# Kernel tuning notes

Measured on AMD Instinct MI355X. Metric: run time of the kernel, lower is better.

The kernel has to match this reference:

```python
import jax, jax.numpy as jnp
import numpy as np
import math

_PI = math.pi

@jax.custom_vjp
def atan_spike(h):
    # Heaviside forward, ATan surrogate (alpha=2.0) backward
    return (h >= 0).astype(h.dtype)

def _atan_fwd(h):
    return (h >= 0).astype(h.dtype), h

def _atan_bwd(h, g):
    # d/dh [ (1/pi) atan(pi*h) + 1/2 ] = 1 / (1 + (pi*h)^2)
    return (g / (1.0 + (_PI * h) ** 2),)

atan_spike.defvjp(_atan_fwd, _atan_bwd)

def plif_scan(x, alpha, v_th):
    # x: [T, ...]; PLIF: v += alpha*(x - v); spike; hard reset to 0
    a = alpha.reshape(())
    def step(v, xt):
        v = v + a * (xt - v)
        s = atan_spike(v - v_th)
        v = v * (1.0 - s)
        return v, s
    v0 = jnp.zeros_like(x[0])
    _, spikes = jax.lax.scan(step, v0, x)
    return spikes

def setup_inputs() -> dict:
    key = jax.random.key(0)
    k1, k2, k3 = jax.random.split(key, 3)
    T, B, N, D, H = 4, 8, 1024, 512, 2048
    x = jax.random.normal(k1, (T, B, N, D), dtype=jnp.float32)
    W1 = jax.random.normal(k2, (H, D), dtype=jnp.float32) * (1.0 / math.sqrt(D))
    W2 = jax.random.normal(k3, (D, H), dtype=jnp.float32) * (1.0 / math.sqrt(H))
    alpha1 = jnp.full((1,), 0.5, dtype=jnp.float32)  # 1/tau, tau=2.0
    alpha2 = jnp.full((1,), 0.5, dtype=jnp.float32)
    return {"x": x, "W1": W1, "W2": W2, "alpha1": alpha1, "alpha2": alpha2}

def reference(x, W1, W2, alpha1, alpha2):
    V_TH = 1.0
    h = jnp.einsum('tbnd,hd->tbnh', x, W1)      # fc1 (no bias)
    s1 = plif_scan(h, alpha1, V_TH)             # PLIF neuron 1
    y = jnp.einsum('tbnh,dh->tbnd', s1, W2)     # fc2 (no bias)
    s2 = plif_scan(y, alpha2, V_TH)             # PLIF neuron 2
    return s2
```

## Files before the change

### kernel.cpp

```cpp
#include <hip/hip_runtime.h>

#define T_  4
#define BN_ 8192
#define D_  512
#define H_  2048

typedef float f4 __attribute__((ext_vector_type(4)));
typedef float f32x4 __attribute__((ext_vector_type(4)));
typedef _Float16 f16x8 __attribute__((ext_vector_type(8)));

__device__ __forceinline__ void split8(const f4 u0, const f4 u1, f16x8& hi, f16x8& lo) {
#pragma unroll
    for (int i = 0; i < 4; ++i) {
        _Float16 a = (_Float16)u0[i]; hi[i]     = a; lo[i]     = (_Float16)(u0[i] - (float)a);
        _Float16 b = (_Float16)u1[i]; hi[4 + i] = b; lo[4 + i] = (_Float16)(u1[i] - (float)b);
    }
}

__device__ __forceinline__ void spikes4_to_f16(unsigned b, unsigned& lo, unsigned& hi) {
    const unsigned p0 = (b & 0xFFu) | ((b & 0xFF00u) << 8);
    const unsigned p1 = ((b >> 16) & 0xFFu) | ((b >> 8) & 0xFF0000u);
    lo = p0 * 0x3C00u;
    hi = p1 * 0x3C00u;
}

__device__ __forceinline__ void glds16(const void* g, void* l) {
    __builtin_amdgcn_global_load_lds((const __attribute__((address_space(1))) unsigned int*)g,
                                     (__attribute__((address_space(3))) unsigned int*)l, 16, 0, 0);
}

__global__ __launch_bounds__(256)
void k_split(const float* __restrict__ x, _Float16* __restrict__ xs)
{
    const int b     = blockIdx.x;
    const int t     = b & 3;
    const int k0B   = (b >> 2) & 15;
    const int bnB64 = b >> 6;
    const int kg    = threadIdx.x & 3;
    const int row64 = threadIdx.x >> 2;

    const float* src = x + ((size_t)t * BN_ + bnB64 * 64 + row64) * D_ + k0B * 32 + kg * 8;
    const f4 u0 = *(const f4*)src;
    const f4 u1 = *(const f4*)(src + 4);
    f16x8 hi, lo;
    split8(u0, u1, hi, lo);

    const int bnB32 = bnB64 * 2 + (row64 >> 5);
    const int r     = row64 & 31;
    const size_t base = (size_t)(bnB32 * 16 + k0B) * 8192 + t * 2048;
    *(f16x8*)&xs[base +        kg * 256 + r * 8] = hi;
    *(f16x8*)&xs[base + 1024 + kg * 256 + r * 8] = lo;
}

__global__ __launch_bounds__(256)
void k_splitW(const float* __restrict__ W1, _Float16* __restrict__ w1s)
{
    const int gid = blockIdx.x * 256 + threadIdx.x;
    const int col = gid & 127;
    const int kg  = (gid >> 7) & 3;
    const int kb  = (gid >> 9) & 15;
    const int h0b = gid >> 13;

    const float* src = W1 + (size_t)(h0b * 128 + col) * D_ + kb * 32 + kg * 8;
    const f4 u0 = *(const f4*)src;
    const f4 u1 = *(const f4*)(src + 4);
    f16x8 hi, lo;
    split8(u0, u1, hi, lo);

    const size_t base = (size_t)(h0b * 16 + kb) * 8192;
    *(f16x8*)&w1s[base +        kg * 1024 + col * 8] = hi;
    *(f16x8*)&w1s[base + 4096 + kg * 1024 + col * 8] = lo;
}

__global__ __launch_bounds__(256)
void k_splitW2(const float* __restrict__ W2, _Float16* __restrict__ w2s)
{
    const int gid = blockIdx.x * 256 + threadIdx.x;
    const int col = gid & 127;
    const int kg  = (gid >> 7) & 3;
    const int kb  = (gid >> 9) & 63;
    const int d0b = gid >> 15;

    const float* src = W2 + (size_t)(d0b * 128 + col) * H_ + kb * 32 + kg * 8;
    const f4 u0 = *(const f4*)src;
    const f4 u1 = *(const f4*)(src + 4);
    f16x8 hi, lo;
    split8(u0, u1, hi, lo);

    const size_t base = (size_t)(d0b * 64 + kb) * 8192;
    *(f16x8*)&w2s[base +        kg * 1024 + col * 8] = hi;
    *(f16x8*)&w2s[base + 4096 + kg * 1024 + col * 8] = lo;
}

__global__ __launch_bounds__(256, 4)
void k_fc1b(const _Float16* __restrict__ xs, const _Float16* __restrict__ w1s,
            const float* __restrict__ alphap, unsigned char* __restrict__ s1)
{
    __shared__ _Float16 Ab[2][T_][2][4][32][8];

    const int tid  = threadIdx.x;
    const int lane = tid & 63;
    const int w    = tid >> 6;
    const int wc   = w * 32;

    const int gid   = blockIdx.x;
    const int panel = gid >> 8;
    const int h0i   = (gid >> 4) & 15;
    const int bnL   = gid & 15;
    const int bnB   = panel * 16 + bnL;
    const int bn0   = bnB * 32;
    const int h0    = h0i * 128;

    const int l15 = lane & 15;
    const int kgl = lane >> 4;
    const int lq  = kgl * 4;

    const float a1v = alphap[0];

    f32x4 acc[T_][2][2];
#pragma unroll
    for (int t = 0; t < T_; ++t)
#pragma unroll
        for (int m = 0; m < 2; ++m)
#pragma unroll
            for (int n = 0; n < 2; ++n) acc[t][m][n] = (f32x4){0.f, 0.f, 0.f, 0.f};

    const char* xbase = (const char*)xs + (size_t)bnB * 16 * 16384;
    const _Float16* bl = w1s + (size_t)h0i * (16 * 8192)
                             + (size_t)kgl * 1024 + (size_t)(wc + l15) * 8;

#define FC1_GLDS(BUF, KB)                                                        \
    {                                                                            \
        const char* cb_ = xbase + (size_t)(KB) * 16384;                          \
        _Float16* lA_ = &Ab[BUF][0][0][0][0][0];                                 \
        _Pragma("unroll")                                                        \
        for (int i_ = 0; i_ < 4; ++i_) {                                         \
            const int s_ = i_ * 4 + w;                                           \
            glds16(cb_ + s_ * 1024 + lane * 16, lA_ + s_ * 512);                 \
        }                                                                        \
    }

#define FC1_BLOAD(KB, B0, B1)                                                    \
    {                                                                            \
        const _Float16* bp_ = bl + (size_t)(KB) * 8192;                          \
        B0[0] = *(const f16x8*)(bp_);                                            \
        B0[1] = *(const f16x8*)(bp_ + 128);                                      \
        B1[0] = *(const f16x8*)(bp_ + 4096);                                     \
        B1[1] = *(const f16x8*)(bp_ + 4096 + 128);                               \
    }

#define FC1_COMPUTE(BUF, B0, B1)                                                 \
    _Pragma("unroll")                                                            \
    for (int t_ = 0; t_ < T_; ++t_)                                              \
        _Pragma("unroll")                                                        \
        for (int m_ = 0; m_ < 2; ++m_) {                                         \
            const f16x8 a0_ = *(const f16x8*)&Ab[BUF][t_][0][kgl][m_ * 16 + l15][0]; \
            const f16x8 a1_ = *(const f16x8*)&Ab[BUF][t_][1][kgl][m_ * 16 + l15][0]; \
            _Pragma("unroll")                                                    \
            for (int n_ = 0; n_ < 2; ++n_) {                                     \
                acc[t_][m_][n_] = __builtin_amdgcn_mfma_f32_16x16x32_f16(a0_, B0[n_], acc[t_][m_][n_], 0, 0, 0); \
                acc[t_][m_][n_] = __builtin_amdgcn_mfma_f32_16x16x32_f16(a0_, B1[n_], acc[t_][m_][n_], 0, 0, 0); \
                acc[t_][m_][n_] = __builtin_amdgcn_mfma_f32_16x16x32_f16(a1_, B0[n_], acc[t_][m_][n_], 0, 0, 0); \
            }                                                                    \
        }

    f16x8 bA0[2], bA1[2], bB0[2], bB1[2];

    FC1_BLOAD(0, bA0, bA1)
    __builtin_amdgcn_sched_barrier(0);
    FC1_GLDS(0, 0)

#pragma unroll 1
    for (int it = 0; it < 8; ++it) {
        const int kb = 2 * it;
        __builtin_amdgcn_s_barrier();
        FC1_BLOAD(kb + 1, bB0, bB1)
        __builtin_amdgcn_sched_barrier(0);
        FC1_GLDS(1, kb + 1)
        asm volatile("s_waitcnt vmcnt(8)" ::: "memory");
        __builtin_amdgcn_sched_barrier(0);
        FC1_COMPUTE(0, bA0, bA1)
        __builtin_amdgcn_s_barrier();
        if (it < 7) {
            FC1_BLOAD(kb + 2, bA0, bA1)
            __builtin_amdgcn_sched_barrier(0);
            FC1_GLDS(0, kb + 2)
            asm volatile("s_waitcnt vmcnt(8)" ::: "memory");
        } else {
            asm volatile("s_waitcnt vmcnt(0)" ::: "memory");
        }
        __builtin_amdgcn_sched_barrier(0);
        FC1_COMPUTE(1, bB0, bB1)
    }

#pragma unroll
    for (int m = 0; m < 2; ++m)
#pragma unroll
        for (int n = 0; n < 2; ++n)
#pragma unroll
            for (int q = 0; q < 4; ++q) {
                float v = 0.f;
#pragma unroll
                for (int t = 0; t < T_; ++t) {
                    v = v + a1v * (acc[t][m][n][q] - v);
                    const bool sp = (v >= 1.0f);
                    s1[((size_t)t * BN_ + bn0 + m * 16 + lq + q) * H_ +
                       (h0 + wc + n * 16 + l15)] = sp ? (unsigned char)1 : (unsigned char)0;
                    if (sp) v = 0.f;
                }
            }
}

__global__ __launch_bounds__(256, 2)
void k_fc2b(const unsigned char* __restrict__ s1, const _Float16* __restrict__ w2s,
            const float* __restrict__ alphap, float* __restrict__ out)
{
    __shared__ _Float16 A2[2][T_][4][64][8];

    const int tid  = threadIdx.x;
    const int lane = tid & 63;
    const int w    = tid >> 6;
    const int wr   = (w >> 1) * 32;
    const int wc   = (w & 1) * 64;
    const int bn0  = blockIdx.x * 64;
    const int d0i  = blockIdx.y;
    const int d0   = d0i * 128;

    const int l15 = lane & 15;
    const int kgl = lane >> 4;
    const int lq  = kgl * 4;

    const int at   = w;
    const int arow = lane;

    const float a2v = alphap[0];

    f32x4 acc[T_][2][4];
#pragma unroll
    for (int t = 0; t < T_; ++t)
#pragma unroll
        for (int m = 0; m < 2; ++m)
#pragma unroll
            for (int n = 0; n < 4; ++n) acc[t][m][n] = (f32x4){0.f, 0.f, 0.f, 0.f};

    const unsigned char* ap = s1 + ((size_t)at * BN_ + bn0 + arow) * H_;
    const _Float16* bl = w2s + (size_t)d0i * (64 * 8192)
                             + (size_t)kgl * 1024 + (size_t)(wc + l15) * 8;

#define FC2_ACONV_WRITE(BUF, R0, R1)                                             \
    {                                                                            \
        unsigned v_[8];                                                          \
        spikes4_to_f16(R0.x, v_[0], v_[1]); spikes4_to_f16(R0.y, v_[2], v_[3]);  \
        spikes4_to_f16(R0.z, v_[4], v_[5]); spikes4_to_f16(R0.w, v_[6], v_[7]);  \
        *(uint4*)&A2[BUF][at][0][arow][0] = *(const uint4*)&v_[0];               \
        *(uint4*)&A2[BUF][at][1][arow][0] = *(const uint4*)&v_[4];               \
        spikes4_to_f16(R1.x, v_[0], v_[1]); spikes4_to_f16(R1.y, v_[2], v_[3]);  \
        spikes4_to_f16(R1.z, v_[4], v_[5]); spikes4_to_f16(R1.w, v_[6], v_[7]);  \
        *(uint4*)&A2[BUF][at][2][arow][0] = *(const uint4*)&v_[0];               \
        *(uint4*)&A2[BUF][at][3][arow][0] = *(const uint4*)&v_[4];               \
    }

#define FC2_BLOAD(KB, B0, B1)                                                    \
    {                                                                            \
        const _Float16* bp_ = bl + (size_t)(KB) * 8192;                          \
        _Pragma("unroll")                                                        \
        for (int n_ = 0; n_ < 4; ++n_) {                                         \
            B0[n_] = *(const f16x8*)(bp_ + n_ * 128);                            \
            B1[n_] = *(const f16x8*)(bp_ + 4096 + n_ * 128);                     \
        }                                                                        \
    }

    f16x8 bc0[4], bc1[4], bpA0[4], bpA1[4];

    {
        const uint4 r0 = *(const uint4*)(ap);
        const uint4 r1 = *(const uint4*)(ap + 16);
        FC2_ACONV_WRITE(0, r0, r1)
        FC2_BLOAD(0, bc0, bc1)
    }
    __syncthreads();

    int cur = 0;
    for (int kb = 0; kb < 64; ++kb) {
        uint4 r0, r1;
        if (kb < 63) {
            r0 = *(const uint4*)(ap + (kb + 1) * 32);
            r1 = *(const uint4*)(ap + (kb + 1) * 32 + 16);
            FC2_BLOAD(kb + 1, bpA0, bpA1)
        }

#pragma unroll
        for (int t = 0; t < T_; ++t)
#pragma unroll
            for (int m = 0; m < 2; ++m) {
                const f16x8 af = *(const f16x8*)&A2[cur][t][kgl][wr + m * 16 + l15][0];
#pragma unroll
                for (int n = 0; n < 4; ++n) {
                    acc[t][m][n] = __builtin_amdgcn_mfma_f32_16x16x32_f16(af, bc0[n], acc[t][m][n], 0, 0, 0);
                    acc[t][m][n] = __builtin_amdgcn_mfma_f32_16x16x32_f16(af, bc1[n], acc[t][m][n], 0, 0, 0);
                }
            }

        if (kb < 63) {
            FC2_ACONV_WRITE(cur ^ 1, r0, r1)
        }
        __syncthreads();
        if (kb < 63) {
#pragma unroll
            for (int n = 0; n < 4; ++n) { bc0[n] = bpA0[n]; bc1[n] = bpA1[n]; }
        }
        cur ^= 1;
    }

#pragma unroll
    for (int m = 0; m < 2; ++m)
#pragma unroll
        for (int n = 0; n < 4; ++n)
#pragma unroll
            for (int q = 0; q < 4; ++q) {
                float v = 0.f;
#pragma unroll
                for (int t = 0; t < T_; ++t) {
                    v = v + a2v * (acc[t][m][n][q] - v);
                    const bool sp = (v >= 1.0f);
                    out[((size_t)t * BN_ + bn0 + wr + m * 16 + lq + q) * D_ +
                        (d0 + wc + n * 16 + l15)] = sp ? 1.0f : 0.0f;
                    if (sp) v = 0.f;
                }
            }
}

__global__ __launch_bounds__(256, 2)
void k_fc2(const unsigned char* __restrict__ s1, const float* __restrict__ W2,
           const float* __restrict__ alphap, float* __restrict__ out)
{
    __shared__ _Float16 A2[2][4][4][64][8];
    __shared__ _Float16 B2[2][2][4][128][8];

    const int tid  = threadIdx.x;
    const int lane = tid & 63;
    const int w    = tid >> 6;
    const int wr   = (w >> 1) * 32;
    const int wc   = (w & 1) * 64;
    const int bn0  = blockIdx.x * 64;
    const int d0   = blockIdx.y * 128;

    const int l15 = lane & 15;
    const int kgl = lane >> 4;
    const int lq  = kgl * 4;

    const int bcol = tid & 127;
    const int bkh  = tid >> 7;
    const int at   = tid >> 6;
    const int arow = lane;

    const float a2v = alphap[0];

    f32x4 acc[T_][2][4];
#pragma unroll
    for (int t = 0; t < T_; ++t)
#pragma unroll
        for (int m = 0; m < 2; ++m)
#pragma unroll
            for (int n = 0; n < 4; ++n) acc[t][m][n] = (f32x4){0.f, 0.f, 0.f, 0.f};

    const unsigned char* ap = s1 + ((size_t)at * BN_ + bn0 + arow) * H_;
    const float*         wp0 = W2 + (size_t)(d0 + bcol) * H_ + bkh * 16;

    {
        const uint4 r0 = *(const uint4*)(ap);
        const uint4 r1 = *(const uint4*)(ap + 16);
        unsigned v[8];
        spikes4_to_f16(r0.x, v[0], v[1]); spikes4_to_f16(r0.y, v[2], v[3]);
        spikes4_to_f16(r0.z, v[4], v[5]); spikes4_to_f16(r0.w, v[6], v[7]);
        *(uint4*)&A2[0][at][0][arow][0] = *(const uint4*)&v[0];
        *(uint4*)&A2[0][at][1][arow][0] = *(const uint4*)&v[4];
        spikes4_to_f16(r1.x, v[0], v[1]); spikes4_to_f16(r1.y, v[2], v[3]);
        spikes4_to_f16(r1.z, v[4], v[5]); spikes4_to_f16(r1.w, v[6], v[7]);
        *(uint4*)&A2[0][at][2][arow][0] = *(const uint4*)&v[0];
        *(uint4*)&A2[0][at][3][arow][0] = *(const uint4*)&v[4];

        const f4 w0 = *(const f4*)wp0, w1 = *(const f4*)(wp0 + 4);
        const f4 w2 = *(const f4*)(wp0 + 8), w3 = *(const f4*)(wp0 + 12);
        f16x8 hA, lA, hB, lB;
        split8(w0, w1, hA, lA); split8(w2, w3, hB, lB);
        *(f16x8*)&B2[0][0][2 * bkh][bcol][0]     = hA;
        *(f16x8*)&B2[0][0][2 * bkh + 1][bcol][0] = hB;
        *(f16x8*)&B2[0][1][2 * bkh][bcol][0]     = lA;
        *(f16x8*)&B2[0][1][2 * bkh + 1][bcol][0] = lB;
    }
    __syncthreads();

    int cur = 0;
    for (int kb = 0; kb < 64; ++kb) {
        uint4 r0, r1; f4 w0, w1, w2, w3;
        if (kb < 63) {
            r0 = *(const uint4*)(ap + (kb + 1) * 32);
            r1 = *(const uint4*)(ap + (kb + 1) * 32 + 16);
            const float* wp = wp0 + (kb + 1) * 32;
            w0 = *(const f4*)wp;       w1 = *(const f4*)(wp + 4);
            w2 = *(const f4*)(wp + 8); w3 = *(const f4*)(wp + 12);
        }

        f16x8 bf0[4], bf1[4];
#pragma unroll
        for (int n = 0; n < 4; ++n) {
            bf0[n] = *(const f16x8*)&B2[cur][0][kgl][wc + n * 16 + l15][0];
            bf1[n] = *(const f16x8*)&B2[cur][1][kgl][wc + n * 16 + l15][0];
        }
#pragma unroll
        for (int t = 0; t < T_; ++t)
#pragma unroll
            for (int m = 0; m < 2; ++m) {
                const f16x8 af = *(const f16x8*)&A2[cur][t][kgl][wr + m * 16 + l15][0];
#pragma unroll
                for (int n = 0; n < 4; ++n) {
                    acc[t][m][n] = __builtin_amdgcn_mfma_f32_16x16x32_f16(af, bf0[n], acc[t][m][n], 0, 0, 0);
                    acc[t][m][n] = __builtin_amdgcn_mfma_f32_16x16x32_f16(af, bf1[n], acc[t][m][n], 0, 0, 0);
                }
            }

        if (kb < 63) {
            unsigned v[8];
            spikes4_to_f16(r0.x, v[0], v[1]); spikes4_to_f16(r0.y, v[2], v[3]);
            spikes4_to_f16(r0.z, v[4], v[5]); spikes4_to_f16(r0.w, v[6], v[7]);
            *(uint4*)&A2[cur ^ 1][at][0][arow][0] = *(const uint4*)&v[0];
            *(uint4*)&A2[cur ^ 1][at][1][arow][0] = *(const uint4*)&v[4];
            spikes4_to_f16(r1.x, v[0], v[1]); spikes4_to_f16(r1.y, v[2], v[3]);
            spikes4_to_f16(r1.z, v[4], v[5]); spikes4_to_f16(r1.w, v[6], v[7]);
            *(uint4*)&A2[cur ^ 1][at][2][arow][0] = *(const uint4*)&v[0];
            *(uint4*)&A2[cur ^ 1][at][3][arow][0] = *(const uint4*)&v[4];

            f16x8 hA, lA, hB, lB;
            split8(w0, w1, hA, lA); split8(w2, w3, hB, lB);
            *(f16x8*)&B2[cur ^ 1][0][2 * bkh][bcol][0]     = hA;
            *(f16x8*)&B2[cur ^ 1][0][2 * bkh + 1][bcol][0] = hB;
            *(f16x8*)&B2[cur ^ 1][1][2 * bkh][bcol][0]     = lA;
            *(f16x8*)&B2[cur ^ 1][1][2 * bkh + 1][bcol][0] = lB;
        }
        __syncthreads();
        cur ^= 1;
    }

#pragma unroll
    for (int m = 0; m < 2; ++m)
#pragma unroll
        for (int n = 0; n < 4; ++n)
#pragma unroll
            for (int q = 0; q < 4; ++q) {
                float v = 0.f;
#pragma unroll
                for (int t = 0; t < T_; ++t) {
                    v = v + a2v * (acc[t][m][n][q] - v);
                    const bool sp = (v >= 1.0f);
                    out[((size_t)t * BN_ + bn0 + wr + m * 16 + lq + q) * D_ +
                        (d0 + wc + n * 16 + l15)] = sp ? 1.0f : 0.0f;
                    if (sp) v = 0.f;
                }
            }
}

extern "C" void kernel_launch(void* const* d_in, const int* in_sizes, int n_in,
                              void* d_out, int out_size, void* d_ws, size_t ws_size,
                              hipStream_t stream) {
    const float* x      = (const float*)d_in[0];
    const float* W1     = (const float*)d_in[1];
    const float* W2     = (const float*)d_in[2];
    const float* alpha1 = (const float*)d_in[3];
    const float* alpha2 = (const float*)d_in[4];
    float* out = (float*)d_out;

    unsigned char* s1 = (unsigned char*)d_ws;
    _Float16* xs = (_Float16*)d_out;
    const size_t S1_BYTES  = (size_t)T_ * BN_ * H_;
    const size_t W1S_BYTES = (size_t)H_ * D_ * 2 * sizeof(_Float16);
    const size_t W2S_BYTES = (size_t)D_ * H_ * 2 * sizeof(_Float16);

    k_split<<<dim3(8192), dim3(256), 0, stream>>>(x, xs);

    _Float16* w1s = (_Float16*)((char*)d_ws + S1_BYTES);
    k_splitW<<<dim3(512), dim3(256), 0, stream>>>(W1, w1s);
    k_fc1b<<<dim3(4096), dim3(256), 0, stream>>>(xs, w1s, alpha1, s1);

    if (ws_size >= S1_BYTES + W1S_BYTES + W2S_BYTES) {
        _Float16* w2s = (_Float16*)((char*)d_ws + S1_BYTES + W1S_BYTES);
        k_splitW2<<<dim3(512), dim3(256), 0, stream>>>(W2, w2s);
        k_fc2b<<<dim3(128, 4), dim3(256), 0, stream>>>(s1, w2s, alpha2, out);
    } else {
        k_fc2<<<dim3(128, 4), dim3(256), 0, stream>>>(s1, W2, alpha2, out);
    }
}
```

Before: 300.8 us.

## Deepen fc1 software pipeline to three-stage LDS and register buffering

Changes the fc1 GEMM main loop from double buffering to triple buffering. The LDS A tile gains a third stage and B fragments get three register sets, so loads run two k-blocks ahead with vmcnt waits of 16. This aims to hide more global-load latency behind the MFMA work. In exchange it uses more LDS and registers, and launch bounds drop to 3 waves per SIMD, which lowers occupancy.

```diff
diff --git a/kernel.cpp b/kernel.cpp
--- a/kernel.cpp
+++ b/kernel.cpp
@@ -92,11 +92,11 @@
     *(f16x8*)&w2s[base + 4096 + kg * 1024 + col * 8] = lo;
 }
 
-__global__ __launch_bounds__(256, 4)
+__global__ __launch_bounds__(256, 3)
 void k_fc1b(const _Float16* __restrict__ xs, const _Float16* __restrict__ w1s,
             const float* __restrict__ alphap, unsigned char* __restrict__ s1)
 {
-    __shared__ _Float16 Ab[2][T_][2][4][32][8];
+    __shared__ _Float16 Ab[3][T_][2][4][32][8];
 
     const int tid  = threadIdx.x;
     const int lane = tid & 63;
@@ -164,34 +164,44 @@
             }                                                                    \
         }
 
-    f16x8 bA0[2], bA1[2], bB0[2], bB1[2];
-
-    FC1_BLOAD(0, bA0, bA1)
-    __builtin_amdgcn_sched_barrier(0);
+#define FC1_SB __builtin_amdgcn_sched_barrier(0);
+#define FC1_WAIT(N) asm volatile("s_waitcnt vmcnt(" #N ")" ::: "memory");
+
+#define FC1_PHASE(P, SC0, SC1, SP0, SP1, BUFC, BUFP, PRE, WN)                    \
+    __builtin_amdgcn_s_barrier();                                                \
+    FC1_SB                                                                       \
+    if (PRE) {                                                                   \
+        FC1_BLOAD((P) + 2, SP0, SP1)                                             \
+        FC1_SB                                                                   \
+        FC1_GLDS(BUFP, (P) + 2)                                                  \
+        FC1_SB                                                                   \
+    }                                                                            \
+    FC1_WAIT(WN)                                                                 \
+    FC1_SB                                                                       \
+    FC1_COMPUTE(BUFC, SC0, SC1)
+
+    f16x8 b0A[2], b0B[2], b1A[2], b1B[2], b2A[2], b2B[2];
+
+    FC1_BLOAD(0, b0A, b0B)
+    FC1_SB
     FC1_GLDS(0, 0)
+    FC1_SB
+    FC1_BLOAD(1, b1A, b1B)
+    FC1_SB
+    FC1_GLDS(1, 1)
+    FC1_SB
 
 #pragma unroll 1
-    for (int it = 0; it < 8; ++it) {
-        const int kb = 2 * it;
-        __builtin_amdgcn_s_barrier();
-        FC1_BLOAD(kb + 1, bB0, bB1)
-        __builtin_amdgcn_sched_barrier(0);
-        FC1_GLDS(1, kb + 1)
-        asm volatile("s_waitcnt vmcnt(8)" ::: "memory");
-        __builtin_amdgcn_sched_barrier(0);
-        FC1_COMPUTE(0, bA0, bA1)
-        __builtin_amdgcn_s_barrier();
-        if (it < 7) {
-            FC1_BLOAD(kb + 2, bA0, bA1)
-            __builtin_amdgcn_sched_barrier(0);
-            FC1_GLDS(0, kb + 2)
-            asm volatile("s_waitcnt vmcnt(8)" ::: "memory");
-        } else {
-            asm volatile("s_waitcnt vmcnt(0)" ::: "memory");
-        }
-        __builtin_amdgcn_sched_barrier(0);
-        FC1_COMPUTE(1, bB0, bB1)
-    }
+    for (int i = 0; i < 4; ++i) {
+        const int p = 3 * i;
+        FC1_PHASE(p,     b0A, b0B, b2A, b2B, 0, 2, 1, 16)
+        FC1_PHASE(p + 1, b1A, b1B, b0A, b0B, 1, 0, 1, 16)
+        FC1_PHASE(p + 2, b2A, b2B, b1A, b1B, 2, 1, 1, 16)
+    }
+    FC1_PHASE(12, b0A, b0B, b2A, b2B, 0, 2, 1, 16)
+    FC1_PHASE(13, b1A, b1B, b0A, b0B, 1, 0, 1, 16)
+    FC1_PHASE(14, b2A, b2B, b0A, b0B, 2, 0, 0, 8)
+    FC1_PHASE(15, b0A, b0B, b0A, b0B, 0, 0, 0, 0)
 
 #pragma unroll
     for (int m = 0; m < 2; ++m)
```

After: 297.3 us. About the same (-1.1%).

## Replace LDS-direct loads in fc1 with register-staged double buffering and MFMA priority

Applied to the files above, without the earlier changes.

The fc1 kernel stops using global_load_lds DMA with hand-placed waitcnts. It now prefetches the next A tile into registers, computes on the current LDS buffer, then writes the prefetched data to the alternate buffer, with one __syncthreads per k-step. The launch-bounds occupancy hint drops from 4 to 2 to leave room for the extra registers, and s_setprio raises wave priority around the MFMA blocks in both fc1 and fc2. This trades the direct-to-LDS path for a simpler, compiler-scheduled pipeline, at the cost of more VGPRs, possibly lower occupancy, and extra LDS write instructions.

```diff
diff --git a/kernel.cpp b/kernel.cpp
--- a/kernel.cpp
+++ b/kernel.cpp
@@ -22,11 +22,6 @@
     const unsigned p1 = ((b >> 16) & 0xFFu) | ((b >> 8) & 0xFF0000u);
     lo = p0 * 0x3C00u;
     hi = p1 * 0x3C00u;
-}
-
-__device__ __forceinline__ void glds16(const void* g, void* l) {
-    __builtin_amdgcn_global_load_lds((const __attribute__((address_space(1))) unsigned int*)g,
-                                     (__attribute__((address_space(3))) unsigned int*)l, 16, 0, 0);
 }
 
 __global__ __launch_bounds__(256)
@@ -92,8 +87,8 @@
     *(f16x8*)&w2s[base + 4096 + kg * 1024 + col * 8] = lo;
 }
 
-__global__ __launch_bounds__(256, 4)
-void k_fc1b(const _Float16* __restrict__ xs, const _Float16* __restrict__ w1s,
+__global__ __launch_bounds__(256, 2)
+void k_fc1d(const _Float16* __restrict__ xs, const _Float16* __restrict__ w1s,
             const float* __restrict__ alphap, unsigned char* __restrict__ s1)
 {
     __shared__ _Float16 Ab[2][T_][2][4][32][8];
@@ -129,15 +124,24 @@
     const _Float16* bl = w1s + (size_t)h0i * (16 * 8192)
                              + (size_t)kgl * 1024 + (size_t)(wc + l15) * 8;
 
-#define FC1_GLDS(BUF, KB)                                                        \
+    _Float16* const aw = &Ab[0][0][0][0][0][0];
+
+#define FC1_ALOAD(KB, R)                                                         \
     {                                                                            \
-        const char* cb_ = xbase + (size_t)(KB) * 16384;                          \
-        _Float16* lA_ = &Ab[BUF][0][0][0][0][0];                                 \
-        _Pragma("unroll")                                                        \
-        for (int i_ = 0; i_ < 4; ++i_) {                                         \
-            const int s_ = i_ * 4 + w;                                           \
-            glds16(cb_ + s_ * 1024 + lane * 16, lA_ + s_ * 512);                 \
-        }                                                                        \
+        const char* cb_ = xbase + (size_t)(KB) * 16384 + tid * 64;               \
+        R[0] = *(const uint4*)(cb_);                                             \
+        R[1] = *(const uint4*)(cb_ + 16);                                        \
+        R[2] = *(const uint4*)(cb_ + 32);                                        \
+        R[3] = *(const uint4*)(cb_ + 48);                                        \
+    }
+
+#define FC1_AWRITE(BUF, R)                                                       \
+    {                                                                            \
+        _Float16* lp_ = aw + (BUF) * 8192 + tid * 32;                            \
+        *(uint4*)(lp_)      = R[0];                                              \
+        *(uint4*)(lp_ + 8)  = R[1];                                              \
+        *(uint4*)(lp_ + 16) = R[2];                                              \
+        *(uint4*)(lp_ + 24) = R[3];                                              \
     }
 
 #define FC1_BLOAD(KB, B0, B1)                                                    \
@@ -150,6 +154,7 @@
     }
 
 #define FC1_COMPUTE(BUF, B0, B1)                                                 \
+    __builtin_amdgcn_s_setprio(1);                                               \
     _Pragma("unroll")                                                            \
     for (int t_ = 0; t_ < T_; ++t_)                                              \
         _Pragma("unroll")                                                        \
@@ -162,35 +167,36 @@
                 acc[t_][m_][n_] = __builtin_amdgcn_mfma_f32_16x16x32_f16(a0_, B1[n_], acc[t_][m_][n_], 0, 0, 0); \
                 acc[t_][m_][n_] = __builtin_amdgcn_mfma_f32_16x16x32_f16(a1_, B0[n_], acc[t_][m_][n_], 0, 0, 0); \
             }                                                                    \
-        }
-
-    f16x8 bA0[2], bA1[2], bB0[2], bB1[2];
-
-    FC1_BLOAD(0, bA0, bA1)
-    __builtin_amdgcn_sched_barrier(0);
-    FC1_GLDS(0, 0)
-
+        }                                                                        \
+    __builtin_amdgcn_s_setprio(0);
+
+    f16x8 bc0[2], bc1[2], bp0[2], bp1[2];
+    uint4 ar[4];
+
+    FC1_ALOAD(0, ar)
+    FC1_BLOAD(0, bc0, bc1)
+    FC1_AWRITE(0, ar)
+    __syncthreads();
+
+    int cur = 0;
 #pragma unroll 1
-    for (int it = 0; it < 8; ++it) {
-        const int kb = 2 * it;
-        __builtin_amdgcn_s_barrier();
-        FC1_BLOAD(kb + 1, bB0, bB1)
-        __builtin_amdgcn_sched_barrier(0);
-        FC1_GLDS(1, kb + 1)
-        asm volatile("s_waitcnt vmcnt(8)" ::: "memory");
-        __builtin_amdgcn_sched_barrier(0);
-        FC1_COMPUTE(0, bA0, bA1)
-        __builtin_amdgcn_s_barrier();
-        if (it < 7) {
-            FC1_BLOAD(kb + 2, bA0, bA1)
-            __builtin_amdgcn_sched_barrier(0);
-            FC1_GLDS(0, kb + 2)
-            asm volatile("s_waitcnt vmcnt(8)" ::: "memory");
-        } else {
-            asm volatile("s_waitcnt vmcnt(0)" ::: "memory");
-        }
-        __builtin_amdgcn_sched_barrier(0);
-        FC1_COMPUTE(1, bB0, bB1)
+    for (int kb = 0; kb < 16; ++kb) {
+        if (kb < 15) {
+            FC1_ALOAD(kb + 1, ar)
+            FC1_BLOAD(kb + 1, bp0, bp1)
+        }
+
+        FC1_COMPUTE(cur, bc0, bc1)
+
+        if (kb < 15) {
+            FC1_AWRITE(cur ^ 1, ar)
+        }
+        __syncthreads();
+        if (kb < 15) {
+#pragma unroll
+            for (int n = 0; n < 2; ++n) { bc0[n] = bp0[n]; bc1[n] = bp1[n]; }
+        }
+        cur ^= 1;
     }
 
 #pragma unroll
@@ -289,6 +295,7 @@
             FC2_BLOAD(kb + 1, bpA0, bpA1)
         }
 
+        __builtin_amdgcn_s_setprio(1);
 #pragma unroll
         for (int t = 0; t < T_; ++t)
 #pragma unroll
@@ -300,6 +307,7 @@
                     acc[t][m][n] = __builtin_amdgcn_mfma_f32_16x16x32_f16(af, bc1[n], acc[t][m][n], 0, 0, 0);
                 }
             }
+        __builtin_amdgcn_s_setprio(0);
 
         if (kb < 63) {
             FC2_ACONV_WRITE(cur ^ 1, r0, r1)
@@ -480,7 +488,7 @@
 
     _Float16* w1s = (_Float16*)((char*)d_ws + S1_BYTES);
     k_splitW<<<dim3(512), dim3(256), 0, stream>>>(W1, w1s);
-    k_fc1b<<<dim3(4096), dim3(256), 0, stream>>>(xs, w1s, alpha1, s1);
+    k_fc1d<<<dim3(4096), dim3(256), 0, stream>>>(xs, w1s, alpha1, s1);
 
     if (ws_size >= S1_BYTES + W1S_BYTES + W2S_BYTES) {
         _Float16* w2s = (_Float16*)((char*)d_ws + S1_BYTES + W1S_BYTES);
```

Result: slower. 439.7 us (+46.2%).
